# Kernel tuning notes

Measured on AMD Instinct MI355X. Metric: run time of the kernel, lower is better.

## Reference

```python
import jax, jax.numpy as jnp
import numpy as np

B, N = 8, 50000
NB, NA, NT, NI, NC = 60000, 120000, 180000, 20000, 1500000


def _term_index(key, n_terms, arity, n_atoms):
    # distinct atom indices per term (avoids degenerate zero-length vectors)
    k1, k2 = jax.random.split(key)
    base = jax.random.randint(k1, (n_terms,), 0, n_atoms)
    cols = [base]
    for a in range(arity - 1):
        off = jax.random.randint(jax.random.fold_in(k2, a), (n_terms,), 1, n_atoms)
        cols.append((base + off + a) % n_atoms)
    return jnp.stack(cols, axis=1).astype(jnp.int32)


def setup_inputs() -> dict:
    key = jax.random.key(0)
    ks = jax.random.split(key, 24)
    u = lambda k, s, lo, hi: jax.random.uniform(k, s, jnp.float32, lo, hi)
    coords = jax.random.normal(ks[0], (B, N, 3), jnp.float32) * 10.0
    return dict(
        coords=coords,
        bond_index=_term_index(ks[1], NB, 2, N),
        bond_rest_length=u(ks[2], (NB,), 1.0, 2.0),
        bond_force_constant=u(ks[3], (NB,), 200.0, 800.0),
        angle_index=_term_index(ks[4], NA, 3, N),
        angle_force_constant=u(ks[5], (NA,), 50.0, 300.0),
        angle_c0=u(ks[6], (NA,), 0.5, 2.0),
        angle_c1=u(ks[7], (NA,), -1.0, 1.0),
        angle_c2=u(ks[8], (NA,), -1.0, 1.0),
        torsion_index=_term_index(ks[9], NT, 4, N),
        torsion_force_constant=u(ks[10], (NT,), 1.0, 20.0),
        torsion_order=jax.random.randint(ks[11], (NT,), 1, 7).astype(jnp.int32),
        torsion_cos_term=jnp.where(jax.random.bernoulli(ks[12], 0.5, (NT,)), 1.0, -1.0).astype(jnp.float32),
        inversion_index=_term_index(ks[13], NI, 4, N),
        inversion_force_constant=u(ks[14], (NI,), 1.0, 40.0),
        inversion_c0=u(ks[15], (NI,), 0.5, 1.5),
        inversion_c1=u(ks[16], (NI,), -1.0, 1.0),
        inversion_c2=u(ks[17], (NI,), -1.0, 1.0),
        nonbond_index=_term_index(ks[18], NC, 2, N),
        vdw_minimum=u(ks[19], (NC,), 3.0, 4.0),
        vdw_well_depth=u(ks[20], (NC,), 0.01, 0.2),
        vdw_threshold_sq=jnp.square(u(ks[21], (NC,), 10.0, 30.0)),
    )


def _uff_energy(coords, bond_index, bond_rest_length, bond_force_constant,
                angle_index, angle_force_constant, angle_c0, angle_c1, angle_c2,
                torsion_index, torsion_force_constant, torsion_order, torsion_cos_term,
                inversion_index, inversion_force_constant, inversion_c0, inversion_c1, inversion_c2,
                nonbond_index, vdw_minimum, vdw_well_depth, vdw_threshold_sq):
    take = lambda idx: jnp.take(coords, idx, axis=1)  # (B, P, 3)

    # ---- bond stretch: 0.5 * k * (|r_ij| - r0)^2 ----
    d = take(bond_index[:, 0]) - take(bond_index[:, 1])
    dist = jnp.sqrt(jnp.sum(d * d, -1))
    e_bond = jnp.sum(0.5 * bond_force_constant * jnp.square(dist - bond_rest_length), -1)

    # ---- angle bend (general cosine expansion, order == 0 branch) ----
    p1, p2, p3 = take(angle_index[:, 0]), take(angle_index[:, 1]), take(angle_index[:, 2])
    v1, v2 = p1 - p2, p3 - p2
    dot = jnp.sum(v1 * v2, -1)
    inv = jax.lax.rsqrt(jnp.maximum(jnp.sum(v1 * v1, -1) * jnp.sum(v2 * v2, -1), 1e-24))
    ct = jnp.clip(dot * inv, -0.999999, 0.999999)
    cs = ct * ct
    ss = jnp.maximum(1.0 - cs, 1e-12)
    e_angle = jnp.sum(angle_force_constant * (angle_c0 + angle_c1 * ct + angle_c2 * (cs - ss)), -1)

    # ---- torsion: 0.5 * V * (1 - cos_term * cos(n * phi)) ----
    q1, q2, q3, q4 = (take(torsion_index[:, a]) for a in range(4))
    b1, b2, b3 = q2 - q1, q3 - q2, q4 - q3
    n1 = jnp.cross(b1, b2)
    n2 = jnp.cross(b2, b3)
    cn = jnp.sum(n1 * n2, -1) * jax.lax.rsqrt(
        jnp.maximum(jnp.sum(n1 * n1, -1) * jnp.sum(n2 * n2, -1), 1e-24))
    phi = jnp.arccos(jnp.clip(cn, -0.999999, 0.999999))
    n_f = torsion_order.astype(coords.dtype)
    e_tor = jnp.sum(0.5 * torsion_force_constant * (1.0 - torsion_cos_term * jnp.cos(n_f * phi)), -1)

    # ---- inversion (Wilson angle): K*(c0 + c1*sinY + c2*(2*sinY^2 - 1)), central atom = col 1 ----
    cA = take(inversion_index[:, 1])
    rji = take(inversion_index[:, 0]) - cA
    rjk = take(inversion_index[:, 2]) - cA
    rjl = take(inversion_index[:, 3]) - cA
    nrm = jnp.cross(rji, rjk)
    cosY = jnp.sum(nrm * rjl, -1) * jax.lax.rsqrt(
        jnp.maximum(jnp.sum(nrm * nrm, -1) * jnp.sum(rjl * rjl, -1), 1e-24))
    cosY = jnp.clip(cosY, -0.999999, 0.999999)
    sinY = jnp.sqrt(jnp.maximum(1.0 - cosY * cosY, 0.0))
    e_inv = jnp.sum(inversion_force_constant * (inversion_c0 + inversion_c1 * sinY
                                                + inversion_c2 * (2.0 * sinY * sinY - 1.0)), -1)

    # ---- vdW LJ on radius-graph candidates: D*((R/r)^12 - 2*(R/r)^6) within cutoff ----
    dnb = take(nonbond_index[:, 0]) - take(nonbond_index[:, 1])
    d2 = jnp.sum(dnb * dnb, -1)
    within = d2 <= vdw_threshold_sq  # pair selection done under no_grad in the original
    x2 = jnp.square(vdw_minimum) / jnp.maximum(d2, 1e-12)
    x6 = x2 * x2 * x2
    e_pair = vdw_well_depth * (x6 * x6 - 2.0 * x6)
    e_vdw = jnp.sum(jnp.where(within, e_pair, 0.0), -1)

    return e_bond + e_angle + e_tor + e_inv + e_vdw  # (B,)


def reference(coords, bond_index, bond_rest_length, bond_force_constant,
              angle_index, angle_force_constant, angle_c0, angle_c1, angle_c2,
              torsion_index, torsion_force_constant, torsion_order, torsion_cos_term,
              inversion_index, inversion_force_constant, inversion_c0, inversion_c1, inversion_c2,
              nonbond_index, vdw_minimum, vdw_well_depth, vdw_threshold_sq):
    return _uff_energy(coords, bond_index, bond_rest_length, bond_force_constant,
                       angle_index, angle_force_constant, angle_c0, angle_c1, angle_c2,
                       torsion_index, torsion_force_constant, torsion_order, torsion_cos_term,
                       inversion_index, inversion_force_constant, inversion_c0, inversion_c1, inversion_c2,
                       nonbond_index, vdw_minimum, vdw_well_depth, vdw_threshold_sq)
```

## Files before the change

### kernel.cpp

```cpp
#include <hip/hip_runtime.h>

#define TPB 256
#define NWAVE (TPB / 64)
#define GRID_MAIN 2048

typedef int vi2 __attribute__((ext_vector_type(2)));
typedef int vi4 __attribute__((ext_vector_type(4)));

struct SegInfo {
    int cb, ca, ct, ci, cl;
    int NB, NA, NT, NI, NC;
    int N;
};

__device__ __forceinline__ float clamp1(float x) {
    return fminf(fmaxf(x, -0.999999f), 0.999999f);
}

__device__ __forceinline__ float ntf(const float* p) { return __builtin_nontemporal_load(p); }
__device__ __forceinline__ int   nti(const int* p)   { return __builtin_nontemporal_load(p); }

template <bool USE_WS>
__device__ __forceinline__ float4 loadC(const float4* __restrict__ cw,
                                        const float* __restrict__ coords,
                                        int N, int atom, int b) {
    if (USE_WS) {
        return cw[((size_t)atom << 3) + b];
    } else {
        const float* sp = coords + ((size_t)b * N + atom) * 3;
        return make_float4(sp[0], sp[1], sp[2], 0.f);
    }
}

__global__ void __launch_bounds__(TPB) transpose_coords(const float* __restrict__ coords,
                                                        float4* __restrict__ cw,
                                                        float* __restrict__ out, int N) {
    const int a = blockIdx.x * TPB + threadIdx.x;
    if (blockIdx.x == 0 && threadIdx.x < 8) out[threadIdx.x] = 0.f;
    if (a >= N) return;
#pragma unroll
    for (int b = 0; b < 8; b++) {
        const float* sp = coords + ((size_t)b * N + a) * 3;
        cw[((size_t)a << 3) + b] = make_float4(ntf(sp), ntf(sp + 1), ntf(sp + 2), 0.f);
    }
}

__device__ __forceinline__ void stage(
    int c, const SegInfo& s, int lane,
    const int* __restrict__ bidx, const float* __restrict__ br0, const float* __restrict__ bk,
    const int* __restrict__ aidx, const float* __restrict__ ak,
    const float* __restrict__ ac0, const float* __restrict__ ac1, const float* __restrict__ ac2,
    const int* __restrict__ tidx, const float* __restrict__ tk,
    const int* __restrict__ tord, const float* __restrict__ tcos,
    const int* __restrict__ iidx, const float* __restrict__ ik,
    const float* __restrict__ ic0, const float* __restrict__ ic1, const float* __restrict__ ic2,
    const int* __restrict__ nidx, const float* __restrict__ vmin,
    const float* __restrict__ vdep, const float* __restrict__ vthr,
    int4& ri, float4& rp)
{
    if (c < s.cb) {
        const int u = min(c * 64 + lane, s.NB - 1);
        const vi2 ij = __builtin_nontemporal_load((const vi2*)bidx + u);
        ri = make_int4(ij.x, ij.y, 0, 0);
        rp = make_float4(ntf(br0 + u), ntf(bk + u), 0.f, 0.f);
    } else if (c < s.ca) {
        const int u = min((c - s.cb) * 64 + lane, s.NA - 1);
        ri = make_int4(aidx[3 * u], aidx[3 * u + 1], aidx[3 * u + 2], 0);
        rp = make_float4(ntf(ak + u), ntf(ac0 + u), ntf(ac1 + u), ntf(ac2 + u));
    } else if (c < s.ct) {
        const int u = min((c - s.ca) * 64 + lane, s.NT - 1);
        const vi4 q = __builtin_nontemporal_load((const vi4*)tidx + u);
        ri = make_int4(q.x, q.y, q.z, q.w);
        rp = make_float4(ntf(tk + u), ntf(tcos + u), __int_as_float(nti(tord + u)), 0.f);
    } else if (c < s.ci) {
        const int u = min((c - s.ct) * 64 + lane, s.NI - 1);
        const vi4 q = __builtin_nontemporal_load((const vi4*)iidx + u);
        ri = make_int4(q.x, q.y, q.z, q.w);
        rp = make_float4(ntf(ik + u), ntf(ic0 + u), ntf(ic1 + u), ntf(ic2 + u));
    } else {
        const int u = min((c - s.ci) * 64 + lane, s.NC - 1);
        const vi2 ij = __builtin_nontemporal_load((const vi2*)nidx + u);
        const float R = ntf(vmin + u);
        ri = make_int4(ij.x, ij.y, 0, 0);
        rp = make_float4(R * R, ntf(vdep + u), ntf(vthr + u), 0.f);
    }
}

template <bool USE_WS>
__global__ void __launch_bounds__(TPB, 6) uff_kernel(
    const float* __restrict__ coords, const float4* __restrict__ cw,
    const int* __restrict__ bidx, const float* __restrict__ br0, const float* __restrict__ bk,
    const int* __restrict__ aidx, const float* __restrict__ ak,
    const float* __restrict__ ac0, const float* __restrict__ ac1, const float* __restrict__ ac2,
    const int* __restrict__ tidx, const float* __restrict__ tk,
    const int* __restrict__ tord, const float* __restrict__ tcos,
    const int* __restrict__ iidx, const float* __restrict__ ik,
    const float* __restrict__ ic0, const float* __restrict__ ic1, const float* __restrict__ ic2,
    const int* __restrict__ nidx, const float* __restrict__ vmin,
    const float* __restrict__ vdep, const float* __restrict__ vthr,
    float* __restrict__ out, SegInfo s)
{
    __shared__ int4   sI[NWAVE][64];
    __shared__ float4 sP[NWAVE][64];

    const int tid = threadIdx.x;
    const int lane = tid & 63;
    const int w = tid >> 6;
    const int b = lane & 7;
    const int gw = lane >> 3;
    const int N = s.N;
    float acc = 0.f;

    int4*   mI = sI[w];
    float4* mP = sP[w];

    const int stride = gridDim.x * NWAVE;
    int c = blockIdx.x * NWAVE + w;

    int4 ri; float4 rp;
    if (c < s.cl)
        stage(c, s, lane, bidx, br0, bk, aidx, ak, ac0, ac1, ac2,
              tidx, tk, tord, tcos, iidx, ik, ic0, ic1, ic2,
              nidx, vmin, vdep, vthr, ri, rp);

    while (c < s.cl) {
        mI[lane] = ri;
        mP[lane] = rp;

        int kind, base;
        if (c < s.cb)      { kind = 0; base = c * 64; }
        else if (c < s.ca) { kind = 1; base = (c - s.cb) * 64; }
        else if (c < s.ct) { kind = 2; base = (c - s.ca) * 64; }
        else if (c < s.ci) { kind = 3; base = (c - s.ct) * 64; }
        else               { kind = 4; base = (c - s.ci) * 64; }

        const int cn = c + stride;
        if (cn < s.cl)
            stage(cn, s, lane, bidx, br0, bk, aidx, ak, ac0, ac1, ac2,
                  tidx, tk, tord, tcos, iidx, ik, ic0, ic1, ic2,
                  nidx, vmin, vdep, vthr, ri, rp);

        if (kind == 4) {
#pragma unroll
            for (int jj = 0; jj < 2; jj++) {
                int4 q[4]; float4 p[4], A[4], Bv[4];
#pragma unroll
                for (int j = 0; j < 4; j++) {
                    const int slot = (jj * 4 + j) * 8 + gw;
                    q[j] = mI[slot]; p[j] = mP[slot];
                }
#pragma unroll
                for (int j = 0; j < 4; j++) {
                    A[j]  = loadC<USE_WS>(cw, coords, N, q[j].x, b);
                    Bv[j] = loadC<USE_WS>(cw, coords, N, q[j].y, b);
                }
#pragma unroll
                for (int j = 0; j < 4; j++) {
                    float dx = A[j].x - Bv[j].x, dy = A[j].y - Bv[j].y, dz = A[j].z - Bv[j].z;
                    float d2 = dx * dx + dy * dy + dz * dz;
                    float x2 = p[j].x / fmaxf(d2, 1e-12f);
                    float x6 = x2 * x2 * x2;
                    float e = p[j].y * (x6 * x6 - 2.f * x6);
                    if (base + (jj * 4 + j) * 8 + gw < s.NC && d2 <= p[j].z) acc += e;
                }
            }
        } else if (kind == 0) {
#pragma unroll
            for (int jj = 0; jj < 2; jj++) {
                int4 q[4]; float4 p[4], A[4], Bv[4];
#pragma unroll
                for (int j = 0; j < 4; j++) {
                    const int slot = (jj * 4 + j) * 8 + gw;
                    q[j] = mI[slot]; p[j] = mP[slot];
                }
#pragma unroll
                for (int j = 0; j < 4; j++) {
                    A[j]  = loadC<USE_WS>(cw, coords, N, q[j].x, b);
                    Bv[j] = loadC<USE_WS>(cw, coords, N, q[j].y, b);
                }
#pragma unroll
                for (int j = 0; j < 4; j++) {
                    float dx = A[j].x - Bv[j].x, dy = A[j].y - Bv[j].y, dz = A[j].z - Bv[j].z;
                    float dd = sqrtf(dx * dx + dy * dy + dz * dz) - p[j].x;
                    if (base + (jj * 4 + j) * 8 + gw < s.NB) acc += 0.5f * p[j].y * dd * dd;
                }
            }
        } else if (kind == 1) {
#pragma unroll
            for (int jj = 0; jj < 4; jj++) {
                int4 q[2]; float4 p[2], P[2], Q[2], R[2];
#pragma unroll
                for (int j = 0; j < 2; j++) {
                    const int slot = (jj * 2 + j) * 8 + gw;
                    q[j] = mI[slot]; p[j] = mP[slot];
                }
#pragma unroll
                for (int j = 0; j < 2; j++) {
                    P[j] = loadC<USE_WS>(cw, coords, N, q[j].x, b);
                    Q[j] = loadC<USE_WS>(cw, coords, N, q[j].y, b);
                    R[j] = loadC<USE_WS>(cw, coords, N, q[j].z, b);
                }
#pragma unroll
                for (int j = 0; j < 2; j++) {
                    float ax = P[j].x - Q[j].x, ay = P[j].y - Q[j].y, az = P[j].z - Q[j].z;
                    float bx = R[j].x - Q[j].x, by = R[j].y - Q[j].y, bz = R[j].z - Q[j].z;
                    float dot = ax * bx + ay * by + az * bz;
                    float nn = (ax * ax + ay * ay + az * az) * (bx * bx + by * by + bz * bz);
                    float ct = clamp1(dot * rsqrtf(fmaxf(nn, 1e-24f)));
                    float cs = ct * ct;
                    float sb = fmaxf(1.f - cs, 1e-12f);
                    if (base + (jj * 2 + j) * 8 + gw < s.NA)
                        acc += p[j].x * (p[j].y + p[j].z * ct + p[j].w * (cs - sb));
                }
            }
        } else if (kind == 2) {
#pragma unroll
            for (int jj = 0; jj < 4; jj++) {
                int4 q[2]; float4 p[2], P1[2], P2[2], P3[2], P4[2];
#pragma unroll
                for (int j = 0; j < 2; j++) {
                    const int slot = (jj * 2 + j) * 8 + gw;
                    q[j] = mI[slot]; p[j] = mP[slot];
                }
#pragma unroll
                for (int j = 0; j < 2; j++) {
                    P1[j] = loadC<USE_WS>(cw, coords, N, q[j].x, b);
                    P2[j] = loadC<USE_WS>(cw, coords, N, q[j].y, b);
                    P3[j] = loadC<USE_WS>(cw, coords, N, q[j].z, b);
                    P4[j] = loadC<USE_WS>(cw, coords, N, q[j].w, b);
                }
#pragma unroll
                for (int j = 0; j < 2; j++) {
                    const int ord = __float_as_int(p[j].z);
                    float b1x = P2[j].x - P1[j].x, b1y = P2[j].y - P1[j].y, b1z = P2[j].z - P1[j].z;
                    float b2x = P3[j].x - P2[j].x, b2y = P3[j].y - P2[j].y, b2z = P3[j].z - P2[j].z;
                    float b3x = P4[j].x - P3[j].x, b3y = P4[j].y - P3[j].y, b3z = P4[j].z - P3[j].z;
                    float n1x = b1y * b2z - b1z * b2y;
                    float n1y = b1z * b2x - b1x * b2z;
                    float n1z = b1x * b2y - b1y * b2x;
                    float n2x = b2y * b3z - b2z * b3y;
                    float n2y = b2z * b3x - b2x * b3z;
                    float n2z = b2x * b3y - b2y * b3x;
                    float dot = n1x * n2x + n1y * n2y + n1z * n2z;
                    float nn = (n1x * n1x + n1y * n1y + n1z * n1z) *
                               (n2x * n2x + n2y * n2y + n2z * n2z);
                    float x = clamp1(dot * rsqrtf(fmaxf(nn, 1e-24f)));
                    float Tp = 1.f, Tc = x, res = x;
#pragma unroll
                    for (int kk = 2; kk <= 6; kk++) {
                        float Tn = 2.f * x * Tc - Tp;
                        Tp = Tc; Tc = Tn;
                        if (ord == kk) res = Tn;
                    }
                    if (base + (jj * 2 + j) * 8 + gw < s.NT) acc += 0.5f * p[j].x * (1.f - p[j].y * res);
                }
            }
        } else {
#pragma unroll
            for (int jj = 0; jj < 4; jj++) {
                int4 q[2]; float4 p[2], CA[2], PI[2], PK[2], PL[2];
#pragma unroll
                for (int j = 0; j < 2; j++) {
                    const int slot = (jj * 2 + j) * 8 + gw;
                    q[j] = mI[slot]; p[j] = mP[slot];
                }
#pragma unroll
                for (int j = 0; j < 2; j++) {
                    CA[j] = loadC<USE_WS>(cw, coords, N, q[j].y, b);
                    PI[j] = loadC<USE_WS>(cw, coords, N, q[j].x, b);
                    PK[j] = loadC<USE_WS>(cw, coords, N, q[j].z, b);
                    PL[j] = loadC<USE_WS>(cw, coords, N, q[j].w, b);
                }
#pragma unroll
                for (int j = 0; j < 2; j++) {
                    float jix = PI[j].x - CA[j].x, jiy = PI[j].y - CA[j].y, jiz = PI[j].z - CA[j].z;
                    float jkx = PK[j].x - CA[j].x, jky = PK[j].y - CA[j].y, jkz = PK[j].z - CA[j].z;
                    float lx  = PL[j].x - CA[j].x, ly  = PL[j].y - CA[j].y, lz  = PL[j].z - CA[j].z;
                    float nx = jiy * jkz - jiz * jky;
                    float ny = jiz * jkx - jix * jkz;
                    float nz = jix * jky - jiy * jkx;
                    float dot = nx * lx + ny * ly + nz * lz;
                    float nn = (nx * nx + ny * ny + nz * nz) * (lx * lx + ly * ly + lz * lz);
                    float cosY = clamp1(dot * rsqrtf(fmaxf(nn, 1e-24f)));
                    float sinY = sqrtf(fmaxf(1.f - cosY * cosY, 0.f));
                    if (base + (jj * 2 + j) * 8 + gw < s.NI)
                        acc += p[j].x * (p[j].y + p[j].z * sinY + p[j].w * (2.f * sinY * sinY - 1.f));
                }
            }
        }

        c = cn;
    }

    float v = acc;
    v += __shfl_down(v, 8, 64);
    v += __shfl_down(v, 16, 64);
    v += __shfl_down(v, 32, 64);

    __shared__ float red[NWAVE][8];
    if (lane < 8) red[w][lane] = v;
    __syncthreads();
    if (tid < 8) {
        float ssum = 0.f;
#pragma unroll
        for (int i = 0; i < NWAVE; i++) ssum += red[i][tid];
        atomicAdd(&out[tid], ssum);
    }
}

static inline int cdiv(int a, int b) { return (a + b - 1) / b; }

extern "C" void kernel_launch(void* const* d_in, const int* in_sizes, int n_in,
                              void* d_out, int out_size, void* d_ws, size_t ws_size,
                              hipStream_t stream) {
    const int B = out_size;
    const int NB = in_sizes[2], NA = in_sizes[5], NT = in_sizes[10],
              NI = in_sizes[14], NC = in_sizes[19];
    const int N = in_sizes[0] / (3 * B);

    const float* coords = (const float*)d_in[0];
    const int*   bidx = (const int*)d_in[1];
    const float* br0  = (const float*)d_in[2];
    const float* bk   = (const float*)d_in[3];
    const int*   aidx = (const int*)d_in[4];
    const float* ak   = (const float*)d_in[5];
    const float* ac0  = (const float*)d_in[6];
    const float* ac1  = (const float*)d_in[7];
    const float* ac2  = (const float*)d_in[8];
    const int*   tidx = (const int*)d_in[9];
    const float* tk   = (const float*)d_in[10];
    const int*   tord = (const int*)d_in[11];
    const float* tcos = (const float*)d_in[12];
    const int*   iidx = (const int*)d_in[13];
    const float* ik   = (const float*)d_in[14];
    const float* ic0  = (const float*)d_in[15];
    const float* ic1  = (const float*)d_in[16];
    const float* ic2  = (const float*)d_in[17];
    const int*   nidx = (const int*)d_in[18];
    const float* vmin = (const float*)d_in[19];
    const float* vdep = (const float*)d_in[20];
    const float* vthr = (const float*)d_in[21];

    const size_t cw_bytes = (size_t)N * 8 * sizeof(float4);
    const bool use_ws = ws_size >= cw_bytes;
    float4* cw = (float4*)d_ws;

    if (use_ws) {
        transpose_coords<<<cdiv(N, TPB), TPB, 0, stream>>>(coords, cw, (float*)d_out, N);
    } else {
        hipMemsetAsync(d_out, 0, (size_t)out_size * sizeof(float), stream);
    }

    SegInfo s;
    s.NB = NB; s.NA = NA; s.NT = NT; s.NI = NI; s.NC = NC; s.N = N;
    s.cb = cdiv(NB, 64);
    s.ca = s.cb + cdiv(NA, 64);
    s.ct = s.ca + cdiv(NT, 64);
    s.ci = s.ct + cdiv(NI, 64);
    s.cl = s.ci + cdiv(NC, 64);

    if (use_ws) {
        uff_kernel<true><<<GRID_MAIN, TPB, 0, stream>>>(
            coords, cw, bidx, br0, bk, aidx, ak, ac0, ac1, ac2,
            tidx, tk, tord, tcos, iidx, ik, ic0, ic1, ic2,
            nidx, vmin, vdep, vthr, (float*)d_out, s);
    } else {
        uff_kernel<false><<<GRID_MAIN, TPB, 0, stream>>>(
            coords, cw, bidx, br0, bk, aidx, ak, ac0, ac1, ac2,
            tidx, tk, tord, tcos, iidx, ik, ic0, ic1, ic2,
            nidx, vmin, vdep, vthr, (float*)d_out, s);
    }
}
```

Baseline: 165.9 us.

## Split batch into two halves with separate kernel passes for cache locality

Splits the atom-major coordinate buffer into two halves of four batch entries each and launches the main kernel twice, once per half. Each term is now handled by four lanes instead of eight, so a wave covers 16 terms per step. The intent is to halve the gathered coordinate working set (1.6 MB per half), so random atom gathers hit in cache more often. The cost is that all term index and parameter arrays are streamed twice, and there is an extra kernel launch.

Result: slower. 197.6 us (+19.2%).

```diff
diff --git a/kernel.cpp b/kernel.cpp
--- a/kernel.cpp
+++ b/kernel.cpp
@@ -20,20 +20,21 @@
 __device__ __forceinline__ float ntf(const float* p) { return __builtin_nontemporal_load(p); }
 __device__ __forceinline__ int   nti(const int* p)   { return __builtin_nontemporal_load(p); }
 
-template <bool USE_WS>
-__device__ __forceinline__ float4 loadC(const float4* __restrict__ cw,
+template <bool USE_WS, int HALF>
+__device__ __forceinline__ float4 loadC(const float4* __restrict__ cwH,
                                         const float* __restrict__ coords,
-                                        int N, int atom, int b) {
+                                        int N, int atom, int b4) {
     if (USE_WS) {
-        return cw[((size_t)atom << 3) + b];
+        return cwH[((size_t)atom << 2) + b4];
     } else {
-        const float* sp = coords + ((size_t)b * N + atom) * 3;
+        const float* sp = coords + ((size_t)(HALF * 4 + b4) * N + atom) * 3;
         return make_float4(sp[0], sp[1], sp[2], 0.f);
     }
 }
 
 __global__ void __launch_bounds__(TPB) transpose_coords(const float* __restrict__ coords,
-                                                        float4* __restrict__ cw,
+                                                        float4* __restrict__ cwA,
+                                                        float4* __restrict__ cwB,
                                                         float* __restrict__ out, int N) {
     const int a = blockIdx.x * TPB + threadIdx.x;
     if (blockIdx.x == 0 && threadIdx.x < 8) out[threadIdx.x] = 0.f;
@@ -41,7 +42,9 @@
 #pragma unroll
     for (int b = 0; b < 8; b++) {
         const float* sp = coords + ((size_t)b * N + a) * 3;
-        cw[((size_t)a << 3) + b] = make_float4(ntf(sp), ntf(sp + 1), ntf(sp + 2), 0.f);
+        float4 v = make_float4(ntf(sp), ntf(sp + 1), ntf(sp + 2), 0.f);
+        if (b < 4) cwA[((size_t)a << 2) + b] = v;
+        else       cwB[((size_t)a << 2) + (b - 4)] = v;
     }
 }
 
@@ -86,9 +89,9 @@
     }
 }
 
-template <bool USE_WS>
+template <bool USE_WS, int HALF>
 __global__ void __launch_bounds__(TPB, 6) uff_kernel(
-    const float* __restrict__ coords, const float4* __restrict__ cw,
+    const float* __restrict__ coords, const float4* __restrict__ cwH,
     const int* __restrict__ bidx, const float* __restrict__ br0, const float* __restrict__ bk,
     const int* __restrict__ aidx, const float* __restrict__ ak,
     const float* __restrict__ ac0, const float* __restrict__ ac1, const float* __restrict__ ac2,
@@ -106,8 +109,8 @@
     const int tid = threadIdx.x;
     const int lane = tid & 63;
     const int w = tid >> 6;
-    const int b = lane & 7;
-    const int gw = lane >> 3;
+    const int b4 = lane & 3;
+    const int gwi = lane >> 2;
     const int N = s.N;
     float acc = 0.f;
 
@@ -141,64 +144,58 @@
                   nidx, vmin, vdep, vthr, ri, rp);
 
         if (kind == 4) {
+            int4 q[4]; float4 p[4], A[4], Bv[4];
+#pragma unroll
+            for (int j = 0; j < 4; j++) {
+                const int slot = j * 16 + gwi;
+                q[j] = mI[slot]; p[j] = mP[slot];
+            }
+#pragma unroll
+            for (int j = 0; j < 4; j++) {
+                A[j]  = loadC<USE_WS, HALF>(cwH, coords, N, q[j].x, b4);
+                Bv[j] = loadC<USE_WS, HALF>(cwH, coords, N, q[j].y, b4);
+            }
+#pragma unroll
+            for (int j = 0; j < 4; j++) {
+                float dx = A[j].x - Bv[j].x, dy = A[j].y - Bv[j].y, dz = A[j].z - Bv[j].z;
+                float d2 = dx * dx + dy * dy + dz * dz;
+                float x2 = p[j].x / fmaxf(d2, 1e-12f);
+                float x6 = x2 * x2 * x2;
+                float e = p[j].y * (x6 * x6 - 2.f * x6);
+                if (base + j * 16 + gwi < s.NC && d2 <= p[j].z) acc += e;
+            }
+        } else if (kind == 0) {
+            int4 q[4]; float4 p[4], A[4], Bv[4];
+#pragma unroll
+            for (int j = 0; j < 4; j++) {
+                const int slot = j * 16 + gwi;
+                q[j] = mI[slot]; p[j] = mP[slot];
+            }
+#pragma unroll
+            for (int j = 0; j < 4; j++) {
+                A[j]  = loadC<USE_WS, HALF>(cwH, coords, N, q[j].x, b4);
+                Bv[j] = loadC<USE_WS, HALF>(cwH, coords, N, q[j].y, b4);
+            }
+#pragma unroll
+            for (int j = 0; j < 4; j++) {
+                float dx = A[j].x - Bv[j].x, dy = A[j].y - Bv[j].y, dz = A[j].z - Bv[j].z;
+                float dd = sqrtf(dx * dx + dy * dy + dz * dz) - p[j].x;
+                if (base + j * 16 + gwi < s.NB) acc += 0.5f * p[j].y * dd * dd;
+            }
+        } else if (kind == 1) {
 #pragma unroll
             for (int jj = 0; jj < 2; jj++) {
-                int4 q[4]; float4 p[4], A[4], Bv[4];
-#pragma unroll
-                for (int j = 0; j < 4; j++) {
-                    const int slot = (jj * 4 + j) * 8 + gw;
+                int4 q[2]; float4 p[2], P[2], Q[2], R[2];
+#pragma unroll
+                for (int j = 0; j < 2; j++) {
+                    const int slot = (jj * 2 + j) * 16 + gwi;
                     q[j] = mI[slot]; p[j] = mP[slot];
                 }
 #pragma unroll
-                for (int j = 0; j < 4; j++) {
-                    A[j]  = loadC<USE_WS>(cw, coords, N, q[j].x, b);
-                    Bv[j] = loadC<USE_WS>(cw, coords, N, q[j].y, b);
-                }
-#pragma unroll
-                for (int j = 0; j < 4; j++) {
-                    float dx = A[j].x - Bv[j].x, dy = A[j].y - Bv[j].y, dz = A[j].z - Bv[j].z;
-                    float d2 = dx * dx + dy * dy + dz * dz;
-                    float x2 = p[j].x / fmaxf(d2, 1e-12f);
-                    float x6 = x2 * x2 * x2;
-                    float e = p[j].y * (x6 * x6 - 2.f * x6);
-                    if (base + (jj * 4 + j) * 8 + gw < s.NC && d2 <= p[j].z) acc += e;
-                }
-            }
-        } else if (kind == 0) {
-#pragma unroll
-            for (int jj = 0; jj < 2; jj++) {
-                int4 q[4]; float4 p[4], A[4], Bv[4];
-#pragma unroll
-                for (int j = 0; j < 4; j++) {
-                    const int slot = (jj * 4 + j) * 8 + gw;
-                    q[j] = mI[slot]; p[j] = mP[slot];
-                }
-#pragma unroll
-                for (int j = 0; j < 4; j++) {
-                    A[j]  = loadC<USE_WS>(cw, coords, N, q[j].x, b);
-                    Bv[j] = loadC<USE_WS>(cw, coords, N, q[j].y, b);
-                }
-#pragma unroll
-                for (int j = 0; j < 4; j++) {
-                    float dx = A[j].x - Bv[j].x, dy = A[j].y - Bv[j].y, dz = A[j].z - Bv[j].z;
-                    float dd = sqrtf(dx * dx + dy * dy + dz * dz) - p[j].x;
-                    if (base + (jj * 4 + j) * 8 + gw < s.NB) acc += 0.5f * p[j].y * dd * dd;
-                }
-            }
-        } else if (kind == 1) {
-#pragma unroll
-            for (int jj = 0; jj < 4; jj++) {
-                int4 q[2]; float4 p[2], P[2], Q[2], R[2];
-#pragma unroll
-                for (int j = 0; j < 2; j++) {
-                    const int slot = (jj * 2 + j) * 8 + gw;
-                    q[j] = mI[slot]; p[j] = mP[slot];
-                }
-#pragma unroll
-                for (int j = 0; j < 2; j++) {
-                    P[j] = loadC<USE_WS>(cw, coords, N, q[j].x, b);
-                    Q[j] = loadC<USE_WS>(cw, coords, N, q[j].y, b);
-                    R[j] = loadC<USE_WS>(cw, coords, N, q[j].z, b);
+                for (int j = 0; j < 2; j++) {
+                    P[j] = loadC<USE_WS, HALF>(cwH, coords, N, q[j].x, b4);
+                    Q[j] = loadC<USE_WS, HALF>(cwH, coords, N, q[j].y, b4);
+                    R[j] = loadC<USE_WS, HALF>(cwH, coords, N, q[j].z, b4);
                 }
 #pragma unroll
                 for (int j = 0; j < 2; j++) {
@@ -209,25 +206,25 @@
                     float ct = clamp1(dot * rsqrtf(fmaxf(nn, 1e-24f)));
                     float cs = ct * ct;
                     float sb = fmaxf(1.f - cs, 1e-12f);
-                    if (base + (jj * 2 + j) * 8 + gw < s.NA)
+                    if (base + (jj * 2 + j) * 16 + gwi < s.NA)
                         acc += p[j].x * (p[j].y + p[j].z * ct + p[j].w * (cs - sb));
                 }
             }
         } else if (kind == 2) {
 #pragma unroll
-            for (int jj = 0; jj < 4; jj++) {
+            for (int jj = 0; jj < 2; jj++) {
                 int4 q[2]; float4 p[2], P1[2], P2[2], P3[2], P4[2];
 #pragma unroll
                 for (int j = 0; j < 2; j++) {
-                    const int slot = (jj * 2 + j) * 8 + gw;
+                    const int slot = (jj * 2 + j) * 16 + gwi;
                     q[j] = mI[slot]; p[j] = mP[slot];
                 }
 #pragma unroll
                 for (int j = 0; j < 2; j++) {
-                    P1[j] = loadC<USE_WS>(cw, coords, N, q[j].x, b);
-                    P2[j] = loadC<USE_WS>(cw, coords, N, q[j].y, b);
-                    P3[j] = loadC<USE_WS>(cw, coords, N, q[j].z, b);
-                    P4[j] = loadC<USE_WS>(cw, coords, N, q[j].w, b);
+                    P1[j] = loadC<USE_WS, HALF>(cwH, coords, N, q[j].x, b4);
+                    P2[j] = loadC<USE_WS, HALF>(cwH, coords, N, q[j].y, b4);
+                    P3[j] = loadC<USE_WS, HALF>(cwH, coords, N, q[j].z, b4);
+                    P4[j] = loadC<USE_WS, HALF>(cwH, coords, N, q[j].w, b4);
                 }
 #pragma unroll
                 for (int j = 0; j < 2; j++) {
@@ -252,24 +249,25 @@
                         Tp = Tc; Tc = Tn;
                         if (ord == kk) res = Tn;
                     }
-                    if (base + (jj * 2 + j) * 8 + gw < s.NT) acc += 0.5f * p[j].x * (1.f - p[j].y * res);
+                    if (base + (jj * 2 + j) * 16 + gwi < s.NT)
+                        acc += 0.5f * p[j].x * (1.f - p[j].y * res);
                 }
             }
         } else {
 #pragma unroll
-            for (int jj = 0; jj < 4; jj++) {
+            for (int jj = 0; jj < 2; jj++) {
                 int4 q[2]; float4 p[2], CA[2], PI[2], PK[2], PL[2];
 #pragma unroll
                 for (int j = 0; j < 2; j++) {
-                    const int slot = (jj * 2 + j) * 8 + gw;
+                    const int slot = (jj * 2 + j) * 16 + gwi;
                     q[j] = mI[slot]; p[j] = mP[slot];
                 }
 #pragma unroll
                 for (int j = 0; j < 2; j++) {
-                    CA[j] = loadC<USE_WS>(cw, coords, N, q[j].y, b);
-                    PI[j] = loadC<USE_WS>(cw, coords, N, q[j].x, b);
-                    PK[j] = loadC<USE_WS>(cw, coords, N, q[j].z, b);
-                    PL[j] = loadC<USE_WS>(cw, coords, N, q[j].w, b);
+                    CA[j] = loadC<USE_WS, HALF>(cwH, coords, N, q[j].y, b4);
+                    PI[j] = loadC<USE_WS, HALF>(cwH, coords, N, q[j].x, b4);
+                    PK[j] = loadC<USE_WS, HALF>(cwH, coords, N, q[j].z, b4);
+                    PL[j] = loadC<USE_WS, HALF>(cwH, coords, N, q[j].w, b4);
                 }
 #pragma unroll
                 for (int j = 0; j < 2; j++) {
@@ -283,7 +281,7 @@
                     float nn = (nx * nx + ny * ny + nz * nz) * (lx * lx + ly * ly + lz * lz);
                     float cosY = clamp1(dot * rsqrtf(fmaxf(nn, 1e-24f)));
                     float sinY = sqrtf(fmaxf(1.f - cosY * cosY, 0.f));
-                    if (base + (jj * 2 + j) * 8 + gw < s.NI)
+                    if (base + (jj * 2 + j) * 16 + gwi < s.NI)
                         acc += p[j].x * (p[j].y + p[j].z * sinY + p[j].w * (2.f * sinY * sinY - 1.f));
                 }
             }
@@ -293,18 +291,19 @@
     }
 
     float v = acc;
+    v += __shfl_down(v, 4, 64);
     v += __shfl_down(v, 8, 64);
     v += __shfl_down(v, 16, 64);
     v += __shfl_down(v, 32, 64);
 
-    __shared__ float red[NWAVE][8];
-    if (lane < 8) red[w][lane] = v;
+    __shared__ float red[NWAVE][4];
+    if (lane < 4) red[w][lane] = v;
     __syncthreads();
-    if (tid < 8) {
+    if (tid < 4) {
         float ssum = 0.f;
 #pragma unroll
         for (int i = 0; i < NWAVE; i++) ssum += red[i][tid];
-        atomicAdd(&out[tid], ssum);
+        atomicAdd(&out[HALF * 4 + tid], ssum);
     }
 }
 
@@ -341,12 +340,13 @@
     const float* vdep = (const float*)d_in[20];
     const float* vthr = (const float*)d_in[21];
 
-    const size_t cw_bytes = (size_t)N * 8 * sizeof(float4);
-    const bool use_ws = ws_size >= cw_bytes;
-    float4* cw = (float4*)d_ws;
+    const size_t half_bytes = (size_t)N * 4 * sizeof(float4);
+    const bool use_ws = ws_size >= 2 * half_bytes;
+    float4* cwA = (float4*)d_ws;
+    float4* cwB = (float4*)((char*)d_ws + half_bytes);
 
     if (use_ws) {
-        transpose_coords<<<cdiv(N, TPB), TPB, 0, stream>>>(coords, cw, (float*)d_out, N);
+        transpose_coords<<<cdiv(N, TPB), TPB, 0, stream>>>(coords, cwA, cwB, (float*)d_out, N);
     } else {
         hipMemsetAsync(d_out, 0, (size_t)out_size * sizeof(float), stream);
     }
@@ -360,14 +360,22 @@
     s.cl = s.ci + cdiv(NC, 64);
 
     if (use_ws) {
-        uff_kernel<true><<<GRID_MAIN, TPB, 0, stream>>>(
-            coords, cw, bidx, br0, bk, aidx, ak, ac0, ac1, ac2,
+        uff_kernel<true, 0><<<GRID_MAIN, TPB, 0, stream>>>(
+            coords, cwA, bidx, br0, bk, aidx, ak, ac0, ac1, ac2,
+            tidx, tk, tord, tcos, iidx, ik, ic0, ic1, ic2,
+            nidx, vmin, vdep, vthr, (float*)d_out, s);
+        uff_kernel<true, 1><<<GRID_MAIN, TPB, 0, stream>>>(
+            coords, cwB, bidx, br0, bk, aidx, ak, ac0, ac1, ac2,
             tidx, tk, tord, tcos, iidx, ik, ic0, ic1, ic2,
             nidx, vmin, vdep, vthr, (float*)d_out, s);
     } else {
-        uff_kernel<false><<<GRID_MAIN, TPB, 0, stream>>>(
-            coords, cw, bidx, br0, bk, aidx, ak, ac0, ac1, ac2,
+        uff_kernel<false, 0><<<GRID_MAIN, TPB, 0, stream>>>(
+            coords, cwA, bidx, br0, bk, aidx, ak, ac0, ac1, ac2,
             tidx, tk, tord, tcos, iidx, ik, ic0, ic1, ic2,
             nidx, vmin, vdep, vthr, (float*)d_out, s);
-    }
-}
+        uff_kernel<false, 1><<<GRID_MAIN, TPB, 0, stream>>>(
+            coords, cwB, bidx, br0, bk, aidx, ak, ac0, ac1, ac2,
+            tidx, tk, tord, tcos, iidx, ik, ic0, ic1, ic2,
+            nidx, vmin, vdep, vthr, (float*)d_out, s);
+    }
+}
```
